# Performance work log

Hardware: AMD Instinct MI355X
Metric: run time of the kernel (lower is better)

The kernel has to match this reference:

```python
import jax, jax.numpy as jnp
import numpy as np

EPS = 1e-12

def l2norm(x, axis):
    # torch.nn.functional.normalize: x / max(||x||_2, eps)
    n = jnp.sqrt(jnp.sum(x * x, axis=axis, keepdims=True))
    return x / jnp.maximum(n, EPS)

def setup_inputs() -> dict:
    key = jax.random.key(0)
    k1, k2, k3, k4 = jax.random.split(key, 4)
    B, Cf, H, W = 128, 1024, 16, 16
    n_att, dv = 312, 300
    img = jax.random.normal(k1, (B, Cf, H, W), dtype=jnp.float32)
    # V is initialized from row-normalized w2v embeddings in the module
    V = l2norm(jax.random.normal(k2, (n_att, dv), dtype=jnp.float32), axis=1)
    W1 = jax.random.normal(k3, (dv, Cf), dtype=jnp.float32)
    W2 = jax.random.normal(k4, (dv, Cf), dtype=jnp.float32)
    return {"img": img, "V": V, "W1": W1, "W2": W2}

def reference(img, V, W1, W2):
    vv = l2norm(V, axis=1)                               # [i, v]
    B, Cf, H, Wd = img.shape
    av = l2norm(img.reshape(B, Cf, H * Wd), axis=1)      # [b, f, r]
    Q = vv @ W1                                          # [i, f]
    A = jnp.einsum('if,bfr->bir', Q, av)                 # attention logits
    A = jax.nn.softmax(A, axis=-1)
    F_p = jnp.einsum('bir,bfr->bif', A, av)              # attended features
    Pred_att = jnp.einsum('if,bif->bi', vv @ W2, F_p)
    return Pred_att
```

## Files before the change

kernel.cpp:

```cpp
#include <hip/hip_runtime.h>
#include <math.h>

#define NB   128
#define CF   1024
#define RR   256
#define NA   312
#define DV   300
#define M2   320
#define MT   640
#define NKC  32

typedef _Float16 half8  __attribute__((ext_vector_type(8)));
typedef float float16v  __attribute__((ext_vector_type(16)));

__global__ void k_prep(const float* __restrict__ img, float* __restrict__ invg,
                       _Float16* __restrict__ avT) {
    int rc = blockIdx.x, b = blockIdx.y;
    int r0 = rc * 64;
    int t = threadIdx.x;
    __shared__ __align__(16) char sm[64 * 65 * 4];
    _Float16 (*tile)[65] = (_Float16 (*)[65])sm;
    float    (*ssb)[65]  = (float    (*)[65])sm;
    int fl = t >> 2, cg = t & 3;
    int rl = t >> 2, g  = t & 3;
    float ss[16];
    #pragma unroll
    for (int j = 0; j < 16; ++j) ss[j] = 0.f;

    for (int cc = 0; cc < 16; ++cc) {
        int f0 = cc * 64;
        const float4* p4 = (const float4*)(img + ((size_t)(b * CF + f0 + fl)) * RR + r0 + cg * 16);
        float4 v0 = p4[0], v1 = p4[1], v2 = p4[2], v3 = p4[3];
        __syncthreads();
        float xs[16] = {v0.x, v0.y, v0.z, v0.w, v1.x, v1.y, v1.z, v1.w,
                        v2.x, v2.y, v2.z, v2.w, v3.x, v3.y, v3.z, v3.w};
        #pragma unroll
        for (int j = 0; j < 16; ++j) {
            ss[j] += xs[j] * xs[j];
            tile[fl][cg * 16 + j] = (_Float16)xs[j];
        }
        __syncthreads();
        int kc  = (f0 >> 5) + (g >> 1);
        int kkb = (g & 1) * 16;
        half8 o0, o1;
        #pragma unroll
        for (int j = 0; j < 8; ++j) o0[j] = tile[g * 16 + j][rl];
        #pragma unroll
        for (int j = 0; j < 8; ++j) o1[j] = tile[g * 16 + 8 + j][rl];
        _Float16* q = avT + (((size_t)(b * NKC + kc) * RR + r0 + rl) * 32 + kkb);
        *(half8*)q       = o0;
        *(half8*)(q + 8) = o1;
    }
    __syncthreads();
    #pragma unroll
    for (int j = 0; j < 16; ++j) ssb[fl][cg * 16 + j] = ss[j];
    __syncthreads();
    if (t < 64) {
        float tot = 0.f;
        for (int f2 = 0; f2 < 64; ++f2) tot += ssb[f2][t];
        invg[b * RR + r0 + t] = 1.f / fmaxf(sqrtf(tot), 1e-12f);
    }
}

__global__ void k_q(const float* __restrict__ V, const float* __restrict__ W1,
                    const float* __restrict__ W2, _Float16* __restrict__ Qb) {
    int ib = blockIdx.x;
    int f  = blockIdx.y * 256 + threadIdx.x;
    int i0 = ib * 8;
    int t  = threadIdx.x;
    __shared__ float inv8[8];
    float acc[8] = {0,0,0,0,0,0,0,0};
    bool zero = (ib == 39 || ib == 79);
    int v0 = (ib < 40) ? i0 : i0 - M2;
    if (!zero) {
        int row = t >> 5, l32 = t & 31;
        float s = 0.f;
        for (int v = l32; v < DV; v += 32) { float x = V[(v0 + row) * DV + v]; s += x * x; }
        #pragma unroll
        for (int o = 16; o; o >>= 1) s += __shfl_xor(s, o, 32);
        if (l32 == 0) inv8[row] = 1.f / fmaxf(sqrtf(s), 1e-12f);
        __syncthreads();
        const float* W = (ib < 40) ? W1 : W2;
        for (int v = 0; v < DV; ++v) {
            float wv = W[(size_t)v * CF + f];
            #pragma unroll
            for (int ii = 0; ii < 8; ++ii) acc[ii] += V[(v0 + ii) * DV + v] * wv;
        }
        #pragma unroll
        for (int ii = 0; ii < 8; ++ii) acc[ii] *= inv8[ii];
    }
    #pragma unroll
    for (int ii = 0; ii < 8; ++ii)
        Qb[((size_t)(f >> 5) * MT + (i0 + ii)) * 32 + (f & 31)] = (_Float16)acc[ii];
}

__launch_bounds__(256, 2)
__global__ void k_gemm(const _Float16* __restrict__ Qb, const _Float16* __restrict__ avT,
                       const float* __restrict__ invg, float* __restrict__ out) {
    int lin  = blockIdx.x;
    int xcd  = lin & 7;
    int slot = lin >> 3;
    int bq   = slot / 5;
    int t2   = slot - bq * 5;
    int b    = bq * 8 + xcd;

    int tid = threadIdx.x;
    int lane = tid & 63, w = tid >> 6;
    int nl = lane & 31, kh = lane >> 5;

    int rq1 = t2 * 64 + nl;
    int rq2 = M2 + t2 * 64 + nl;
    int cB  = w * 64 + nl;

    __shared__ float mred[64 * 4];
    __shared__ float mg[64];
    __shared__ float sred[64 * 4];
    __shared__ float dred[64 * 4];

    float16v acc[4][2];
    #pragma unroll
    for (int i = 0; i < 4; ++i)
        #pragma unroll
        for (int j = 0; j < 2; ++j)
            #pragma unroll
            for (int gi = 0; gi < 16; ++gi) acc[i][j][gi] = 0.f;

    half8 aA[8], bA[4], aB[8], bB[4];

    #define LOADF(Aa, Bb, kc_) do {                                              \
        const _Float16* ab = Qb + (size_t)(kc_) * MT * 32 + kh * 8;              \
        Aa[0] = *(const half8*)(ab + (size_t)rq1 * 32);                          \
        Aa[1] = *(const half8*)(ab + (size_t)rq1 * 32 + 16);                     \
        Aa[2] = *(const half8*)(ab + (size_t)rq2 * 32);                          \
        Aa[3] = *(const half8*)(ab + (size_t)rq2 * 32 + 16);                     \
        Aa[4] = *(const half8*)(ab + (size_t)(rq1 + 32) * 32);                   \
        Aa[5] = *(const half8*)(ab + (size_t)(rq1 + 32) * 32 + 16);              \
        Aa[6] = *(const half8*)(ab + (size_t)(rq2 + 32) * 32);                   \
        Aa[7] = *(const half8*)(ab + (size_t)(rq2 + 32) * 32 + 16);              \
        const _Float16* bb = avT + ((size_t)(b * NKC + (kc_)) * RR + cB) * 32 + kh * 8; \
        Bb[0] = *(const half8*)(bb);                                             \
        Bb[1] = *(const half8*)(bb + 16);                                        \
        Bb[2] = *(const half8*)(bb + 32 * 32);                                   \
        Bb[3] = *(const half8*)(bb + 32 * 32 + 16);                              \
    } while (0)

    #define COMP(Aa, Bb) do {                                                    \
        _Pragma("unroll")                                                        \
        for (int ks = 0; ks < 2; ++ks)                                           \
            _Pragma("unroll")                                                    \
            for (int rf = 0; rf < 4; ++rf)                                       \
                _Pragma("unroll")                                                \
                for (int cb = 0; cb < 2; ++cb)                                   \
                    acc[rf][cb] = __builtin_amdgcn_mfma_f32_32x32x16_f16(        \
                        Aa[rf * 2 + ks], Bb[cb * 2 + ks], acc[rf][cb], 0, 0, 0); \
    } while (0)

    LOADF(aA, bA, 0);
    for (int kc = 0; kc < NKC; kc += 2) {
        LOADF(aB, bB, kc + 1);
        COMP(aA, bA);
        if (kc + 2 < NKC) LOADF(aA, bA, kc + 2);
        COMP(aB, bB);
    }
    #undef LOADF
    #undef COMP

    float iv0 = invg[b * RR + w * 64 + nl];
    float iv1 = invg[b * RR + w * 64 + 32 + nl];
    #pragma unroll
    for (int rf = 0; rf < 4; ++rf)
        #pragma unroll
        for (int gi = 0; gi < 16; ++gi) {
            acc[rf][0][gi] *= iv0;
            acc[rf][1][gi] *= iv1;
        }

    float mx[2][16];
    #pragma unroll
    for (int p = 0; p < 2; ++p)
        #pragma unroll
        for (int gi = 0; gi < 16; ++gi)
            mx[p][gi] = fmaxf(acc[2 * p][0][gi], acc[2 * p][1][gi]);
    #pragma unroll
    for (int off = 1; off <= 16; off <<= 1)
        #pragma unroll
        for (int p = 0; p < 2; ++p)
            #pragma unroll
            for (int gi = 0; gi < 16; ++gi)
                mx[p][gi] = fmaxf(mx[p][gi], __shfl_xor(mx[p][gi], off, 64));
    if (nl == 0) {
        #pragma unroll
        for (int p = 0; p < 2; ++p)
            #pragma unroll
            for (int gi = 0; gi < 16; ++gi) {
                int row = (gi & 3) + 8 * (gi >> 2) + 4 * kh;
                mred[(p * 32 + row) * 4 + w] = mx[p][gi];
            }
    }
    __syncthreads();
    if (tid < 64)
        mg[tid] = fmaxf(fmaxf(mred[tid * 4], mred[tid * 4 + 1]),
                        fmaxf(mred[tid * 4 + 2], mred[tid * 4 + 3]));
    __syncthreads();
    float sp[2][16], dp[2][16];
    #pragma unroll
    for (int p = 0; p < 2; ++p)
        #pragma unroll
        for (int gi = 0; gi < 16; ++gi) {
            int row = (gi & 3) + 8 * (gi >> 2) + 4 * kh;
            float m  = mg[p * 32 + row];
            float e0 = __expf(acc[2 * p][0][gi] - m);
            float e1 = __expf(acc[2 * p][1][gi] - m);
            sp[p][gi] = e0 + e1;
            dp[p][gi] = e0 * acc[2 * p + 1][0][gi] + e1 * acc[2 * p + 1][1][gi];
        }
    #pragma unroll
    for (int off = 1; off <= 16; off <<= 1)
        #pragma unroll
        for (int p = 0; p < 2; ++p)
            #pragma unroll
            for (int gi = 0; gi < 16; ++gi) {
                sp[p][gi] += __shfl_xor(sp[p][gi], off, 64);
                dp[p][gi] += __shfl_xor(dp[p][gi], off, 64);
            }
    if (nl == 0) {
        #pragma unroll
        for (int p = 0; p < 2; ++p)
            #pragma unroll
            for (int gi = 0; gi < 16; ++gi) {
                int row = (gi & 3) + 8 * (gi >> 2) + 4 * kh;
                sred[(p * 32 + row) * 4 + w] = sp[p][gi];
                dred[(p * 32 + row) * 4 + w] = dp[p][gi];
            }
    }
    __syncthreads();
    if (tid < 64) {
        float s = sred[tid * 4] + sred[tid * 4 + 1] + sred[tid * 4 + 2] + sred[tid * 4 + 3];
        float d = dred[tid * 4] + dred[tid * 4 + 1] + dred[tid * 4 + 2] + dred[tid * 4 + 3];
        int ig = t2 * 64 + tid;
        if (ig < NA) out[b * NA + ig] = d / s;
    }
}

extern "C" void kernel_launch(void* const* d_in, const int* in_sizes, int n_in,
                              void* d_out, int out_size, void* d_ws, size_t ws_size,
                              hipStream_t stream) {
    const float* img = (const float*)d_in[0];
    const float* V   = (const float*)d_in[1];
    const float* W1  = (const float*)d_in[2];
    const float* W2  = (const float*)d_in[3];
    float* out = (float*)d_out;

    char* ws = (char*)d_ws;
    size_t off = 0;
    float*    invg = (float*)(ws + off);    off += (size_t)NB * RR * 4;
    _Float16* avT  = (_Float16*)(ws + off); off += (size_t)NB * CF * RR * 2;
    _Float16* Qb   = (_Float16*)(ws + off); off += (size_t)NKC * MT * 32 * 2;

    k_prep<<<dim3(4, NB), 256, 0, stream>>>(img, invg, avT);
    k_q<<<dim3(80, 4), 256, 0, stream>>>(V, W1, W2, Qb);
    k_gemm<<<dim3(640), 256, 0, stream>>>(Qb, avT, invg, out);
}
```

Measured before the change: 329.9 us.

## Stage GEMM operand tiles into LDS via async global_load_lds double buffering

Replaces direct per-lane global loads of the Q and avT fragments into registers with asynchronous global-to-LDS copies into double-buffered shared-memory tiles. Each wave then reads its MFMA operands from LDS, and the A-tile row order is rearranged so the accumulator indexing in the softmax epilogue changes accordingly. The intent is to cut redundant global traffic and register pressure, since fragments shared across waves are now loaded once per block. In exchange it adds two block-wide barriers per k-step and 48KB of LDS per block, which may limit the two-blocks-per-CU occupancy target.

```diff
diff --git a/kernel.cpp b/kernel.cpp
--- a/kernel.cpp
+++ b/kernel.cpp
@@ -12,6 +12,12 @@
 
 typedef _Float16 half8  __attribute__((ext_vector_type(8)));
 typedef float float16v  __attribute__((ext_vector_type(16)));
+
+__device__ __forceinline__ void gload16(const void* g, void* l) {
+    __builtin_amdgcn_global_load_lds(
+        (const __attribute__((address_space(1))) void*)g,
+        (__attribute__((address_space(3))) void*)l, 16, 0, 0);
+}
 
 __global__ void k_prep(const float* __restrict__ img, float* __restrict__ invg,
                        _Float16* __restrict__ avT) {
@@ -108,14 +114,15 @@
     int lane = tid & 63, w = tid >> 6;
     int nl = lane & 31, kh = lane >> 5;
 
-    int rq1 = t2 * 64 + nl;
-    int rq2 = M2 + t2 * 64 + nl;
-    int cB  = w * 64 + nl;
-
-    __shared__ float mred[64 * 4];
-    __shared__ float mg[64];
-    __shared__ float sred[64 * 4];
-    __shared__ float dred[64 * 4];
+    __shared__ __align__(16) char smem[49152];
+    _Float16* A0 = (_Float16*)smem;
+    _Float16* A1 = (_Float16*)(smem + 8192);
+    _Float16* B0 = (_Float16*)(smem + 16384);
+    _Float16* B1 = (_Float16*)(smem + 32768);
+    float* mred = (float*)smem;
+    float* mg   = (float*)(smem + 1024);
+    float* sred = (float*)(smem + 1280);
+    float* dred = (float*)(smem + 2304);
 
     float16v acc[4][2];
     #pragma unroll
@@ -125,45 +132,53 @@
             #pragma unroll
             for (int gi = 0; gi < 16; ++gi) acc[i][j][gi] = 0.f;
 
-    half8 aA[8], bA[4], aB[8], bB[4];
-
-    #define LOADF(Aa, Bb, kc_) do {                                              \
-        const _Float16* ab = Qb + (size_t)(kc_) * MT * 32 + kh * 8;              \
-        Aa[0] = *(const half8*)(ab + (size_t)rq1 * 32);                          \
-        Aa[1] = *(const half8*)(ab + (size_t)rq1 * 32 + 16);                     \
-        Aa[2] = *(const half8*)(ab + (size_t)rq2 * 32);                          \
-        Aa[3] = *(const half8*)(ab + (size_t)rq2 * 32 + 16);                     \
-        Aa[4] = *(const half8*)(ab + (size_t)(rq1 + 32) * 32);                   \
-        Aa[5] = *(const half8*)(ab + (size_t)(rq1 + 32) * 32 + 16);              \
-        Aa[6] = *(const half8*)(ab + (size_t)(rq2 + 32) * 32);                   \
-        Aa[7] = *(const half8*)(ab + (size_t)(rq2 + 32) * 32 + 16);              \
-        const _Float16* bb = avT + ((size_t)(b * NKC + (kc_)) * RR + cB) * 32 + kh * 8; \
-        Bb[0] = *(const half8*)(bb);                                             \
-        Bb[1] = *(const half8*)(bb + 16);                                        \
-        Bb[2] = *(const half8*)(bb + 32 * 32);                                   \
-        Bb[3] = *(const half8*)(bb + 32 * 32 + 16);                              \
+    int arow  = tid & 127;
+    int akb0  = tid >> 7;
+    int grow  = (arow < 64) ? (t2 * 64 + arow) : (M2 + t2 * 64 + (arow - 64));
+    size_t a_src0 = (size_t)grow * 32 + akb0 * 8;
+    size_t a_dst0 = ((size_t)akb0 * 128 + arow) * 8;
+    size_t b_src0 = (size_t)tid * 32;
+    size_t b_dst0 = (size_t)tid * 8;
+    const _Float16* bpanel = avT + (size_t)b * NKC * RR * 32;
+
+    #define STAGE(kc_, Ad, Bd) do {                                             \
+        const _Float16* as = Qb + (size_t)(kc_) * MT * 32;                      \
+        gload16(as + a_src0,      (Ad) + a_dst0);                               \
+        gload16(as + a_src0 + 16, (Ad) + a_dst0 + 2048);                        \
+        const _Float16* bs = bpanel + (size_t)(kc_) * RR * 32;                  \
+        gload16(bs + b_src0 + 0 * 8, (Bd) + b_dst0 + 0 * 2048);                 \
+        gload16(bs + b_src0 + 1 * 8, (Bd) + b_dst0 + 1 * 2048);                 \
+        gload16(bs + b_src0 + 2 * 8, (Bd) + b_dst0 + 2 * 2048);                 \
+        gload16(bs + b_src0 + 3 * 8, (Bd) + b_dst0 + 3 * 2048);                 \
     } while (0)
 
-    #define COMP(Aa, Bb) do {                                                    \
-        _Pragma("unroll")                                                        \
-        for (int ks = 0; ks < 2; ++ks)                                           \
-            _Pragma("unroll")                                                    \
-            for (int rf = 0; rf < 4; ++rf)                                       \
-                _Pragma("unroll")                                                \
-                for (int cb = 0; cb < 2; ++cb)                                   \
-                    acc[rf][cb] = __builtin_amdgcn_mfma_f32_32x32x16_f16(        \
-                        Aa[rf * 2 + ks], Bb[cb * 2 + ks], acc[rf][cb], 0, 0, 0); \
+    #define COMPUTE(Al, Bl) do {                                                \
+        _Pragma("unroll")                                                       \
+        for (int ks = 0; ks < 2; ++ks) {                                        \
+            int kb = ks * 2 + kh;                                               \
+            half8 b0f = *(const half8*)((Bl) + ((size_t)kb * 256 + w * 64 + nl) * 8);       \
+            half8 b1f = *(const half8*)((Bl) + ((size_t)kb * 256 + w * 64 + 32 + nl) * 8);  \
+            _Pragma("unroll")                                                   \
+            for (int rf = 0; rf < 4; ++rf) {                                    \
+                half8 af = *(const half8*)((Al) + ((size_t)kb * 128 + rf * 32 + nl) * 8);   \
+                acc[rf][0] = __builtin_amdgcn_mfma_f32_32x32x16_f16(af, b0f, acc[rf][0], 0, 0, 0); \
+                acc[rf][1] = __builtin_amdgcn_mfma_f32_32x32x16_f16(af, b1f, acc[rf][1], 0, 0, 0); \
+            }                                                                   \
+        }                                                                       \
     } while (0)
 
-    LOADF(aA, bA, 0);
+    STAGE(0, A0, B0);
     for (int kc = 0; kc < NKC; kc += 2) {
-        LOADF(aB, bB, kc + 1);
-        COMP(aA, bA);
-        if (kc + 2 < NKC) LOADF(aA, bA, kc + 2);
-        COMP(aB, bB);
-    }
-    #undef LOADF
-    #undef COMP
+        __syncthreads();
+        STAGE(kc + 1, A1, B1);
+        COMPUTE(A0, B0);
+        __syncthreads();
+        if (kc + 2 < NKC) STAGE(kc + 2, A0, B0);
+        COMPUTE(A1, B1);
+    }
+    __syncthreads();
+    #undef STAGE
+    #undef COMPUTE
 
     float iv0 = invg[b * RR + w * 64 + nl];
     float iv1 = invg[b * RR + w * 64 + 32 + nl];
@@ -180,7 +195,7 @@
     for (int p = 0; p < 2; ++p)
         #pragma unroll
         for (int gi = 0; gi < 16; ++gi)
-            mx[p][gi] = fmaxf(acc[2 * p][0][gi], acc[2 * p][1][gi]);
+            mx[p][gi] = fmaxf(acc[p][0][gi], acc[p][1][gi]);
     #pragma unroll
     for (int off = 1; off <= 16; off <<= 1)
         #pragma unroll
@@ -209,10 +224,10 @@
         for (int gi = 0; gi < 16; ++gi) {
             int row = (gi & 3) + 8 * (gi >> 2) + 4 * kh;
             float m  = mg[p * 32 + row];
-            float e0 = __expf(acc[2 * p][0][gi] - m);
-            float e1 = __expf(acc[2 * p][1][gi] - m);
+            float e0 = __expf(acc[p][0][gi] - m);
+            float e1 = __expf(acc[p][1][gi] - m);
             sp[p][gi] = e0 + e1;
-            dp[p][gi] = e0 * acc[2 * p + 1][0][gi] + e1 * acc[2 * p + 1][1][gi];
+            dp[p][gi] = e0 * acc[p + 2][0][gi] + e1 * acc[p + 2][1][gi];
         }
     #pragma unroll
     for (int off = 1; off <= 16; off <<= 1)
```

Measured after the change: 321.5 us. 1.03x faster.
